# Optimization experiments

Hardware: AMD Instinct MI355X
Metric: run time of the kernel (lower is better)

Reference implementation:

```python
import jax, jax.numpy as jnp
import numpy as np

# Fixed hyperparameters from init_kwargs
KH, KW = 3, 3
GRID_SIZE = 5
SPLINE_ORDER = 3
GRID_RANGE = (-1.0, 1.0)


def _make_grid():
    # grid buffer: arange(-k, grid_size + k + 1) * h + grid_range[0], shape (G + 2k + 1,) = (12,)
    h = (GRID_RANGE[1] - GRID_RANGE[0]) / GRID_SIZE
    return (jnp.arange(-SPLINE_ORDER, GRID_SIZE + SPLINE_ORDER + 1, dtype=jnp.float32) * h
            + GRID_RANGE[0])


def _unfold(x):
    # torch.nn.Unfold with kernel (3,3), stride 1, pad 0, dilation 1.
    # Returns (N, C*KH*KW) with channel-major ordering (c, i, j), matching torch.
    B, C, H, W = x.shape
    Ho, Wo = H - KH + 1, W - KW + 1
    cols = [x[:, :, i:i + Ho, j:j + Wo] for i in range(KH) for j in range(KW)]
    p = jnp.stack(cols, axis=2)                    # (B, C, KH*KW, Ho, Wo)
    p = p.reshape(B, C * KH * KW, Ho * Wo)         # (B, in_features, L)
    p = p.transpose(0, 2, 1).reshape(-1, C * KH * KW)  # (B*L, in_features)
    return p, Ho, Wo


def _b_splines(x, grid):
    # x: (N, in_features); grid: (G + 2k + 1,) uniform, shared across features.
    # Returns (N, in_features, G + k) B-spline basis via Cox-de Boor recursion.
    x = x[..., None]  # (N, in, 1)
    bases = ((x >= grid[:-1]) & (x < grid[1:])).astype(x.dtype)  # (N, in, G+2k)
    for k in range(1, SPLINE_ORDER + 1):
        left = (x - grid[: -(k + 1)]) / (grid[k:-1] - grid[: -(k + 1)])
        right = (grid[k + 1:] - x) / (grid[k + 1:] - grid[1:-k])
        bases = left * bases[..., :-1] + right * bases[..., 1:]
    return bases  # (N, in, G + k)


def setup_inputs() -> dict:
    key = jax.random.key(0)
    k1, k2, k3, k4 = jax.random.split(key, 4)
    in_features = 32 * KH * KW  # 288
    out_features = 64
    n_coef = GRID_SIZE + SPLINE_ORDER  # 8
    x = jax.random.normal(k1, (16, 32, 64, 64), dtype=jnp.float32)
    base_weight = jax.random.normal(k2, (out_features, in_features), dtype=jnp.float32) * (1.0 / np.sqrt(in_features))
    spline_weight = jax.random.normal(k3, (out_features, in_features, n_coef), dtype=jnp.float32) * 0.1
    spline_scaler = jax.random.normal(k4, (out_features, in_features), dtype=jnp.float32) * (1.0 / np.sqrt(in_features))
    return {"x": x, "base_weight": base_weight, "spline_weight": spline_weight,
            "spline_scaler": spline_scaler}


def reference(x, base_weight, spline_weight, spline_scaler):
    B = x.shape[0]
    out_features = base_weight.shape[0]
    grid = _make_grid()

    patches, Ho, Wo = _unfold(x)                              # (N, in_features)
    N, in_features = patches.shape

    # KANLinear forward
    base_out = jnp.matmul(jax.nn.relu(patches), base_weight.T)  # (N, out)
    bases = _b_splines(patches, grid)                           # (N, in, G+k)
    scaled_w = spline_weight * spline_scaler[..., None]         # (out, in, G+k)
    spline_out = jnp.matmul(bases.reshape(N, -1), scaled_w.reshape(out_features, -1).T)
    out = base_out + spline_out                                 # (N, out)

    out = out.reshape(B, Ho, Wo, out_features).transpose(0, 3, 1, 2)  # (B, C_out, Ho, Wo)
    return out
```

## Files before the change

kernel.cpp:

```cpp
#include <hip/hip_runtime.h>
#include <stdint.h>

typedef _Float16 half8  __attribute__((ext_vector_type(8)));
typedef float    f32x4  __attribute__((ext_vector_type(4)));
typedef uint32_t u32x4  __attribute__((ext_vector_type(4)));

#define FIN  288
#define NOUT 64
#define LPB  3844
#define KSPL 72
#define SC   200
#define LDSN (31*SC + 2*64 + 64 + 8)


__global__ void prep_bfrag(const float* __restrict__ bw,
                           const float* __restrict__ sw,
                           const float* __restrict__ sc,
                           half8* __restrict__ bfrag) {
  int t = blockIdx.x * 256 + threadIdx.x;
  half8 v;
  int dst;
  if (t < NOUT * FIN) {
    int o = t / FIN;
    int f = t - o * FIN;
    float scale = sc[t];
    const float* p = sw + t * 8;
#pragma unroll
    for (int c = 0; c < 8; ++c) v[c] = (_Float16)(p[c] * scale);
    int ch = f / 9;
    int r  = f - ch * 9;
    int ii = r / 3;
    int jj = r - ii * 3;
    int g  = ch >> 2, q = ch & 3;
    int kt = ii * 24 + jj * 8 + g;
    dst = (kt * 4 + (o >> 4)) * 64 + q * 16 + (o & 15);
  } else {
    int t2 = t - NOUT * FIN;
    int lane = t2 & 63;
    int nf = (t2 >> 6) & 3;
    int ktb = t2 >> 8;
    int o = nf * 16 + (lane & 15);
    int f0 = ktb * 32 + (lane >> 4) * 8;
    const float* p = bw + o * FIN + f0;
#pragma unroll
    for (int c = 0; c < 8; ++c) v[c] = (_Float16)p[c];
    dst = ((KSPL + ktb) * 4 + nf) * 64 + lane;
  }
  bfrag[dst] = v;
}

__device__ inline half8 bspline8(float xv) {
  float u = fmaf(xv, 2.5f, 5.5f);
  float fi = floorf(u);
  int i = (int)fi;
  float t = u - fi, s = 1.0f - t;
  float t2 = t * t, t3 = t2 * t;
  float s2 = s * s, s3 = s2 * s;
  float w3 = t3 * 0.16666667f;
  float w0 = s3 * 0.16666667f;
  float w1 = fmaf(0.5f, t3, -t2) + 0.66666667f;
  float w2 = fmaf(0.5f, s3, -s2) + 0.66666667f;
  uint32_t u01 = __builtin_bit_cast(uint32_t, __builtin_amdgcn_cvt_pkrtz(w0, w1));
  uint32_t u23 = __builtin_bit_cast(uint32_t, __builtin_amdgcn_cvt_pkrtz(w2, w3));
  uint64_t V = (uint64_t)u01 | ((uint64_t)u23 << 32);
  uint32_t vl = (uint32_t)(V << 16);
  u32x4 fr;
#pragma unroll
  for (int q = 0; q < 4; ++q) {
    int d = i - 2 * q;
    uint32_t rr = (uint32_t)(V >> ((48 - 16 * d) & 63));
    fr[q] = ((uint32_t)d <= 3u) ? rr : ((d == 4) ? vl : 0u);
  }
  return __builtin_bit_cast(half8, fr);
}

__global__ __launch_bounds__(256, 4) void kan_main(
    const float* __restrict__ x,
    const half8* __restrict__ bfrag,
    float* __restrict__ out) {
  __shared__ float lx[LDSN];

  const int tid = threadIdx.x;
  const int bid = blockIdx.x;
  const int b  = bid / 62;
  const int ho = bid - b * 62;

  const float* xb = x + b * 131072 + ho * 64;
#pragma unroll
  for (int r = 0; r < 6; ++r) {
    int gid = r * 256 + tid;
    int row = gid >> 4;
    int c   = (row * 683) >> 11;
    int ii  = row - c * 3;
    int colv = (gid & 15) * 4;
    const float4 v = *(const float4*)(xb + c * 4096 + ii * 64 + colv);
    *(float4*)(&lx[c * SC + ii * 64 + colv]) = v;
  }
  __syncthreads();

  const int lane = tid & 63;
  const int wv   = tid >> 6;
  const int quad = lane >> 4;
  const int m16  = lane & 15;
  const int wo   = wv * 16 + m16;

  f32x4 acc[4];
#pragma unroll
  for (int nf = 0; nf < 4; ++nf) acc[nf] = (f32x4){0.f, 0.f, 0.f, 0.f};

  int kt = 0;
#pragma unroll
  for (int ii = 0; ii < 3; ++ii) {
#pragma unroll
    for (int jj = 0; jj < 3; ++jj) {
      const float* lbase = lx + quad * SC + ii * 64 + wo + jj;
#pragma unroll
      for (int g = 0; g < 8; ++g) {
        float xv = lbase[g * (4 * SC)];
        half8 af = bspline8(xv);
#pragma unroll
        for (int nf = 0; nf < 4; ++nf) {
          half8 bf = bfrag[(kt * 4 + nf) * 64 + lane];
          acc[nf] = __builtin_amdgcn_mfma_f32_16x16x32_f16(af, bf, acc[nf], 0, 0, 0);
        }
        ++kt;
      }
    }
  }

#pragma unroll
  for (int kb = 0; kb < 9; ++kb) {
    int f0 = kb * 32 + quad * 8;
    half8 a;
#pragma unroll
    for (int j = 0; j < 8; ++j) {
      int f = f0 + j;
      int c = (f * 57) >> 9;
      int r = f - c * 9;
      int i2 = (r * 11) >> 5;
      int j2 = r - i2 * 3;
      a[j] = (_Float16)fmaxf(lx[c * SC + i2 * 64 + wo + j2], 0.0f);
    }
#pragma unroll
    for (int nf = 0; nf < 4; ++nf) {
      half8 bf = bfrag[((KSPL + kb) * 4 + nf) * 64 + lane];
      acc[nf] = __builtin_amdgcn_mfma_f32_16x16x32_f16(a, bf, acc[nf], 0, 0, 0);
    }
  }

  float* ob = out + b * (NOUT * LPB) + ho * 62;
#pragma unroll
  for (int rg = 0; rg < 4; ++rg) {
    int wo2 = wv * 16 + quad * 4 + rg;
    if (wo2 < 62) {
#pragma unroll
      for (int nf = 0; nf < 4; ++nf) {
        int o = nf * 16 + m16;
        ob[o * LPB + wo2] = acc[nf][rg];
      }
    }
  }
}

extern "C" void kernel_launch(void* const* d_in, const int* in_sizes, int n_in,
                              void* d_out, int out_size, void* d_ws, size_t ws_size,
                              hipStream_t stream) {
  const float* x  = (const float*)d_in[0];
  const float* bw = (const float*)d_in[1];
  const float* sw = (const float*)d_in[2];
  const float* sc = (const float*)d_in[3];
  float* out = (float*)d_out;
  half8* bfrag = (half8*)d_ws;

  prep_bfrag<<<81, 256, 0, stream>>>(bw, sw, sc, bfrag);
  kan_main<<<16 * 62, 256, 0, stream>>>(x, bfrag, out);
}
```

Baseline: 122.3 us.

## Precompute B-spline bases per pixel into workspace instead of recomputing in main kernel

Adds a prep pass that evaluates the cubic B-spline basis once per input pixel and stores it as fp16 fragments in the workspace. The main kernel then loads these fragments from global memory instead of recomputing each basis nine times per output row. The change also reorders the base-weight layout and the LDS layout for the ReLU path, and swizzles the block index order. The cost is a 32 MB fp16 basis buffer that is written and read back through memory, plus a fallback to the old path when the workspace is too small.

Measured after the change: 142.3 us. 1.16x slower.

```diff
diff --git a/kernel.cpp b/kernel.cpp
--- a/kernel.cpp
+++ b/kernel.cpp
@@ -9,14 +9,187 @@
 #define NOUT 64
 #define LPB  3844
 #define KSPL 72
+#define NBF  20736
+#define NBAS (16*64*32*64)
+
 #define SC   200
-#define LDSN (31*SC + 2*64 + 64 + 8)
-
-
-__global__ void prep_bfrag(const float* __restrict__ bw,
-                           const float* __restrict__ sw,
-                           const float* __restrict__ sc,
-                           half8* __restrict__ bfrag) {
+#define LDSN 6432
+
+#define LDSL (31*SC + 2*64 + 64 + 8)
+
+
+__device__ inline half8 bspline8(float xv) {
+  float u = fmaf(xv, 2.5f, 5.5f);
+  float fi = floorf(u);
+  int i = (int)fi;
+  float t = u - fi, s = 1.0f - t;
+  float t2 = t * t, t3 = t2 * t;
+  float s2 = s * s, s3 = s2 * s;
+  float w3 = t3 * 0.16666667f;
+  float w0 = s3 * 0.16666667f;
+  float w1 = fmaf(0.5f, t3, -t2) + 0.66666667f;
+  float w2 = fmaf(0.5f, s3, -s2) + 0.66666667f;
+  uint32_t u01 = __builtin_bit_cast(uint32_t, __builtin_amdgcn_cvt_pkrtz(w0, w1));
+  uint32_t u23 = __builtin_bit_cast(uint32_t, __builtin_amdgcn_cvt_pkrtz(w2, w3));
+  uint64_t V = (uint64_t)u01 | ((uint64_t)u23 << 32);
+  uint32_t vl = (uint32_t)(V << 16);
+  u32x4 fr;
+#pragma unroll
+  for (int q = 0; q < 4; ++q) {
+    int d = i - 2 * q;
+    uint32_t rr = (uint32_t)(V >> ((48 - 16 * d) & 63));
+    fr[q] = ((uint32_t)d <= 3u) ? rr : ((d == 4) ? vl : 0u);
+  }
+  return __builtin_bit_cast(half8, fr);
+}
+
+__global__ __launch_bounds__(256) void prep_all(const float* __restrict__ x,
+                                                const float* __restrict__ bw,
+                                                const float* __restrict__ sw,
+                                                const float* __restrict__ sc,
+                                                half8* __restrict__ ws) {
+  int bid = blockIdx.x;
+  if (bid < 2048) {
+    int t = bid * 256 + threadIdx.x;
+    int w4 = t & 15;
+    int cperm = (t >> 4) & 31;
+    int bh = t >> 9;
+    int c = ((cperm & 7) << 2) | (cperm >> 3);
+    const float4 v = *(const float4*)(x + (bh >> 6) * 131072 + c * 4096 +
+                                      (bh & 63) * 64 + w4 * 4);
+    half8* dst = ws + NBF + (size_t)t * 4;
+    dst[0] = bspline8(v.x);
+    dst[1] = bspline8(v.y);
+    dst[2] = bspline8(v.z);
+    dst[3] = bspline8(v.w);
+  } else {
+    int t = (bid - 2048) * 256 + threadIdx.x;
+    half8 v;
+    int dst;
+    if (t < NOUT * FIN) {
+      int o = t / FIN;
+      int f = t - o * FIN;
+      float scale = sc[t];
+      const float* p = sw + t * 8;
+#pragma unroll
+      for (int c = 0; c < 8; ++c) v[c] = (_Float16)(p[c] * scale);
+      int ch = f / 9;
+      int r  = f - ch * 9;
+      int ii = r / 3;
+      int jj = r - ii * 3;
+      int g  = ch >> 2, q = ch & 3;
+      int kt = ii * 24 + jj * 8 + g;
+      dst = (kt * 4 + (o >> 4)) * 64 + q * 16 + (o & 15);
+    } else {
+      int t2 = t - NOUT * FIN;
+      int lane = t2 & 63;
+      int nf = (t2 >> 6) & 3;
+      int ktb = t2 >> 8;
+      int o = nf * 16 + (lane & 15);
+      int q = lane >> 4;
+      int i2 = ktb / 3;
+      int j2 = ktb - 3 * i2;
+#pragma unroll
+      for (int c0 = 0; c0 < 8; ++c0)
+        v[c0] = (_Float16)bw[o * FIN + 9 * (q * 8 + c0) + 3 * i2 + j2];
+      dst = ((KSPL + ktb) * 4 + nf) * 64 + lane;
+    }
+    ws[dst] = v;
+  }
+}
+
+__global__ __launch_bounds__(256, 4) void kan_main(
+    const float* __restrict__ x,
+    const half8* __restrict__ ws,
+    float* __restrict__ out) {
+  __shared__ float lx[LDSN];
+  const half8* __restrict__ bfrag = ws;
+  const half8* __restrict__ bas   = ws + NBF;
+
+  const int tid = threadIdx.x;
+  int bid0 = blockIdx.x;
+  int bid = (bid0 & 7) * 124 + (bid0 >> 3);
+  const int b  = bid / 62;
+  const int ho = bid - b * 62;
+
+  const float* xb = x + b * 131072 + ho * 64;
+#pragma unroll
+  for (int r = 0; r < 6; ++r) {
+    int gid = r * 256 + tid;
+    int row = gid >> 4;
+    int c   = (row * 683) >> 11;
+    int ii  = row - c * 3;
+    int colv = (gid & 15) * 4;
+    const float4 v = *(const float4*)(xb + c * 4096 + ii * 64 + colv);
+    *(float4*)(&lx[c * SC + (c >> 3) * 8 + ii * 64 + colv]) = v;
+  }
+
+  const int lane = tid & 63;
+  const int wv   = tid >> 6;
+  const int quad = lane >> 4;
+  const int m16  = lane & 15;
+  const int wo   = wv * 16 + m16;
+
+  f32x4 acc[4];
+#pragma unroll
+  for (int nf = 0; nf < 4; ++nf) acc[nf] = (f32x4){0.f, 0.f, 0.f, 0.f};
+
+  const half8* bb = bas + (size_t)((b * 64 + ho) * 32 + quad * 8) * 64 + wo;
+  int kt = 0;
+#pragma unroll
+  for (int ii = 0; ii < 3; ++ii) {
+#pragma unroll
+    for (int jj = 0; jj < 3; ++jj) {
+      const half8* p = bb + ii * 2048 + jj;
+#pragma unroll
+      for (int g = 0; g < 8; ++g) {
+        half8 af = p[g * 64];
+#pragma unroll
+        for (int nf = 0; nf < 4; ++nf) {
+          half8 bf = bfrag[(kt * 4 + nf) * 64 + lane];
+          acc[nf] = __builtin_amdgcn_mfma_f32_16x16x32_f16(af, bf, acc[nf], 0, 0, 0);
+        }
+        ++kt;
+      }
+    }
+  }
+
+  __syncthreads();
+
+  const float* lb = lx + quad * (8 * SC) + quad * 8 + wo;
+#pragma unroll
+  for (int kb = 0; kb < 9; ++kb) {
+    const int i2 = kb / 3;
+    const int j2 = kb - 3 * i2;
+    half8 a;
+#pragma unroll
+    for (int j = 0; j < 8; ++j)
+      a[j] = (_Float16)fmaxf(lb[j * SC + i2 * 64 + j2], 0.0f);
+#pragma unroll
+    for (int nf = 0; nf < 4; ++nf) {
+      half8 bf = bfrag[((KSPL + kb) * 4 + nf) * 64 + lane];
+      acc[nf] = __builtin_amdgcn_mfma_f32_16x16x32_f16(a, bf, acc[nf], 0, 0, 0);
+    }
+  }
+
+  float* ob = out + b * (NOUT * LPB) + ho * 62;
+#pragma unroll
+  for (int rg = 0; rg < 4; ++rg) {
+    int wo2 = wv * 16 + quad * 4 + rg;
+    if (wo2 < 62) {
+#pragma unroll
+      for (int nf = 0; nf < 4; ++nf) {
+        int o = nf * 16 + m16;
+        ob[o * LPB + wo2] = acc[nf][rg];
+      }
+    }
+  }
+}
+
+__global__ void prep_bfrag_legacy(const float* __restrict__ bw,
+                                  const float* __restrict__ sw,
+                                  const float* __restrict__ sc,
+                                  half8* __restrict__ bfrag) {
   int t = blockIdx.x * 256 + threadIdx.x;
   half8 v;
   int dst;
@@ -49,42 +222,15 @@
   bfrag[dst] = v;
 }
 
-__device__ inline half8 bspline8(float xv) {
-  float u = fmaf(xv, 2.5f, 5.5f);
-  float fi = floorf(u);
-  int i = (int)fi;
-  float t = u - fi, s = 1.0f - t;
-  float t2 = t * t, t3 = t2 * t;
-  float s2 = s * s, s3 = s2 * s;
-  float w3 = t3 * 0.16666667f;
-  float w0 = s3 * 0.16666667f;
-  float w1 = fmaf(0.5f, t3, -t2) + 0.66666667f;
-  float w2 = fmaf(0.5f, s3, -s2) + 0.66666667f;
-  uint32_t u01 = __builtin_bit_cast(uint32_t, __builtin_amdgcn_cvt_pkrtz(w0, w1));
-  uint32_t u23 = __builtin_bit_cast(uint32_t, __builtin_amdgcn_cvt_pkrtz(w2, w3));
-  uint64_t V = (uint64_t)u01 | ((uint64_t)u23 << 32);
-  uint32_t vl = (uint32_t)(V << 16);
-  u32x4 fr;
-#pragma unroll
-  for (int q = 0; q < 4; ++q) {
-    int d = i - 2 * q;
-    uint32_t rr = (uint32_t)(V >> ((48 - 16 * d) & 63));
-    fr[q] = ((uint32_t)d <= 3u) ? rr : ((d == 4) ? vl : 0u);
-  }
-  return __builtin_bit_cast(half8, fr);
-}
-
-__global__ __launch_bounds__(256, 4) void kan_main(
+__global__ __launch_bounds__(256, 4) void kan_main_legacy(
     const float* __restrict__ x,
     const half8* __restrict__ bfrag,
     float* __restrict__ out) {
-  __shared__ float lx[LDSN];
-
+  __shared__ float lx[LDSL];
   const int tid = threadIdx.x;
   const int bid = blockIdx.x;
   const int b  = bid / 62;
   const int ho = bid - b * 62;
-
   const float* xb = x + b * 131072 + ho * 64;
 #pragma unroll
   for (int r = 0; r < 6; ++r) {
@@ -97,17 +243,14 @@
     *(float4*)(&lx[c * SC + ii * 64 + colv]) = v;
   }
   __syncthreads();
-
   const int lane = tid & 63;
   const int wv   = tid >> 6;
   const int quad = lane >> 4;
   const int m16  = lane & 15;
   const int wo   = wv * 16 + m16;
-
   f32x4 acc[4];
 #pragma unroll
   for (int nf = 0; nf < 4; ++nf) acc[nf] = (f32x4){0.f, 0.f, 0.f, 0.f};
-
   int kt = 0;
 #pragma unroll
   for (int ii = 0; ii < 3; ++ii) {
@@ -127,7 +270,6 @@
       }
     }
   }
-
 #pragma unroll
   for (int kb = 0; kb < 9; ++kb) {
     int f0 = kb * 32 + quad * 8;
@@ -147,7 +289,6 @@
       acc[nf] = __builtin_amdgcn_mfma_f32_16x16x32_f16(a, bf, acc[nf], 0, 0, 0);
     }
   }
-
   float* ob = out + b * (NOUT * LPB) + ho * 62;
 #pragma unroll
   for (int rg = 0; rg < 4; ++rg) {
@@ -170,8 +311,14 @@
   const float* sw = (const float*)d_in[2];
   const float* sc = (const float*)d_in[3];
   float* out = (float*)d_out;
-  half8* bfrag = (half8*)d_ws;
-
-  prep_bfrag<<<81, 256, 0, stream>>>(bw, sw, sc, bfrag);
-  kan_main<<<16 * 62, 256, 0, stream>>>(x, bfrag, out);
-}
+  half8* ws = (half8*)d_ws;
+
+  const size_t need = (size_t)(NBF + NBAS) * sizeof(half8);
+  if (ws_size >= need) {
+    prep_all<<<2048 + 81, 256, 0, stream>>>(x, bw, sw, sc, ws);
+    kan_main<<<16 * 62, 256, 0, stream>>>(x, ws, out);
+  } else {
+    prep_bfrag_legacy<<<81, 256, 0, stream>>>(bw, sw, sc, ws);
+    kan_main_legacy<<<16 * 62, 256, 0, stream>>>(x, ws, out);
+  }
+}
```
